# Optimization experiments

Measured on AMD Instinct MI355X. Metric: run time of the kernel, lower is better.

The kernel has to match this reference:

```python
import jax, jax.numpy as jnp
import numpy as np
from jax import lax

N_QUBITS = 8
N_BLOCKS = 5

_H = jnp.array([[1.0, 1.0], [1.0, -1.0]], dtype=jnp.complex64) / np.sqrt(2.0).astype(np.float32)
# torchquantum PauliY.diagonalizing_gates = [Z, S, H] applied in order -> matrix H @ S @ Z = H @ diag(1, -1j)
_YROT = _H @ jnp.diag(jnp.array([1.0, -1j], dtype=jnp.complex64))


def apply_gate(st, U, wires):
    # st: [N, 2, 2, ..., 2] (n_qubits trailing axes); U: [2^k, 2^k]
    k = len(wires)
    axes = [w + 1 for w in wires]
    s = jnp.moveaxis(st, axes, list(range(1, k + 1)))
    shp = s.shape
    s = s.reshape(shp[0], 2 ** k, -1)
    s = jnp.einsum('ij,bjr->bir', U, s)
    return jnp.moveaxis(s.reshape(shp), list(range(1, k + 1)), axes)


def u3_mat(th, ph, lam):
    c = jnp.cos(0.5 * th).astype(jnp.complex64)
    s = jnp.sin(0.5 * th).astype(jnp.complex64)
    el = jnp.exp(1j * lam)
    ep = jnp.exp(1j * ph)
    return jnp.stack([jnp.stack([c, -el * s]), jnp.stack([ep * s, ep * el * c])])


def cu3_mat(th, ph, lam):
    M = jnp.eye(4, dtype=jnp.complex64)
    return M.at[2:, 2:].set(u3_mat(th, ph, lam))


def z_expvals(st):
    # <Z_w> for every wire from marginal probabilities
    n = st.ndim - 1
    mag = st.real ** 2 + st.imag ** 2
    outs = []
    for w in range(n):
        axes = tuple(a for a in range(1, n + 1) if a != w + 1)
        p = mag.sum(axes)  # [N, 2]
        outs.append(p[:, 0] - p[:, 1])
    return jnp.stack(outs, axis=1)


def quantum_conv(x, conv_w, conv_b, u3_params, cu3_params, fc_w, fc_b):
    n = N_QUBITS
    B, C, H, W = x.shape
    y = lax.conv_general_dilated(x, conv_w, (1, 1), 'SAME',
                                 dimension_numbers=('NCHW', 'OIHW', 'NCHW'))
    y = y + conv_b[None, :, None, None]
    ang = y.transpose(0, 2, 3, 1).reshape(-1, n)  # [B*H*W, n_qubits]
    Npx = ang.shape[0]
    # RY(theta)|0> encoding: product state of [cos(t/2), sin(t/2)] per wire
    c = jnp.cos(0.5 * ang)
    s = jnp.sin(0.5 * ang)
    st = jnp.stack([c[:, 0], s[:, 0]], axis=1).astype(jnp.complex64)
    for w in range(1, n):
        q = jnp.stack([c[:, w], s[:, w]], axis=1).astype(jnp.complex64)
        st = (st[:, :, None] * q[:, None, :]).reshape(Npx, -1)
    st = st.reshape((Npx,) + (2,) * n)
    # U3CU3Layer0: per block, U3 on each wire then circular CU3 ring
    for b in range(N_BLOCKS):
        for w in range(n):
            st = apply_gate(st, u3_mat(u3_params[b, w, 0], u3_params[b, w, 1], u3_params[b, w, 2]), [w])
        for w in range(n):
            st = apply_gate(st, cu3_mat(cu3_params[b, w, 0], cu3_params[b, w, 1], cu3_params[b, w, 2]), [w, (w + 1) % n])
    # MeasureAll(Z), then MeasureAll(X) and MeasureAll(Y) which MUTATE the device
    # state with their diagonalizing gates (torchquantum semantics)
    mz = z_expvals(st)
    for w in range(n):
        st = apply_gate(st, _H, [w])
    mx = z_expvals(st)
    for w in range(n):
        st = apply_gate(st, _YROT, [w])
    my = z_expvals(st)
    meas = jnp.concatenate([mz, mx, my], axis=1)  # [B*H*W, 3*n]
    out = meas @ fc_w.T + fc_b
    return out.reshape(B, H, W, -1).transpose(0, 3, 1, 2)


def setup_inputs() -> dict:
    key = jax.random.key(0)
    ks = jax.random.split(key, 7)
    n, cin, cout = N_QUBITS, 16, 32
    x = jax.random.normal(ks[0], (4, cin, 64, 64), dtype=jnp.float32)
    conv_w = jax.random.normal(ks[1], (n, cin, 3, 3), dtype=jnp.float32) / np.sqrt(cin * 9)
    conv_b = jax.random.normal(ks[2], (n,), dtype=jnp.float32) * 0.01
    u3_params = jax.random.uniform(ks[3], (N_BLOCKS, n, 3), dtype=jnp.float32, minval=-np.pi, maxval=np.pi)
    cu3_params = jax.random.uniform(ks[4], (N_BLOCKS, n, 3), dtype=jnp.float32, minval=-np.pi, maxval=np.pi)
    fc_w = jax.random.normal(ks[5], (cout, 3 * n), dtype=jnp.float32) / np.sqrt(3 * n)
    fc_b = jax.random.normal(ks[6], (cout,), dtype=jnp.float32) * 0.01
    return {'x': x, 'conv_w': conv_w, 'conv_b': conv_b, 'u3_params': u3_params,
            'cu3_params': cu3_params, 'fc_w': fc_w, 'fc_b': fc_b}


def reference(x, conv_w, conv_b, u3_params, cu3_params, fc_w, fc_b):
    return quantum_conv(x, conv_w, conv_b, u3_params, cu3_params, fc_w, fc_b)
```

## Files before the change

kernel.cpp:

```cpp
#include <hip/hip_runtime.h>

typedef float v2f __attribute__((ext_vector_type(2)));

template<int C>
__device__ __forceinline__ float dppmov(float x) {
  return __int_as_float(__builtin_amdgcn_update_dpp(0, __float_as_int(x), C, 0xF, 0xF, true));
}
template<int IMM>
__device__ __forceinline__ float dswz(float x) {
  return __int_as_float(__builtin_amdgcn_ds_swizzle(__float_as_int(x), IMM));
}
__device__ __forceinline__ float bperm(float x, int a) {
  return __int_as_float(__builtin_amdgcn_ds_bpermute(a, __float_as_int(x)));
}
template<int M>
__device__ __forceinline__ float bfly(float x) {
  if constexpr (M == 1)      return dppmov<0xB1>(x);
  else if constexpr (M == 2) return dppmov<0x4E>(x);
  else if constexpr (M == 3) return dppmov<0x1B>(x);
  else if constexpr (M == 8) return dppmov<0x128>(x);
  else                       return dswz<0x101F>(x);
}
template<int M>
__device__ __forceinline__ v2f bfly2(v2f v) {
  v2f o; o.x = bfly<M>(v.x); o.y = bfly<M>(v.y); return o;
}
__device__ __forceinline__ v2f sp(float s) { v2f v; v.x = s; v.y = s; return v; }
__device__ __forceinline__ v2f vfma(v2f a, v2f b, v2f c) {
  return __builtin_elementwise_fma(a, b, c);
}

template<int M, int CM>
__device__ __forceinline__ void crossG(v2f Sr[16], v2f Si[16],
    const float* g, int lane) {
  const bool hi = (lane & M) != 0;
  float fr, fi, gr, gi;
  if constexpr (CM == 0) {
    fr = hi ? g[6] : g[0]; fi = hi ? g[7] : g[1];
    gr = hi ? g[4] : g[2]; gi = hi ? g[5] : g[3];
  } else {
    const bool ct = (lane & CM) != 0;
    float f0r = hi ? g[6]  : g[0],  f0i = hi ? g[7]  : g[1];
    float g0r = hi ? g[4]  : g[2],  g0i = hi ? g[5]  : g[3];
    float f1r = hi ? g[14] : g[8],  f1i = hi ? g[15] : g[9];
    float g1r = hi ? g[12] : g[10], g1i = hi ? g[13] : g[11];
    fr = ct ? f1r : f0r; fi = ct ? f1i : f0i;
    gr = ct ? g1r : g0r; gi = ct ? g1i : g0i;
  }
  v2f vfr = sp(fr), vfi = sp(fi), vgr = sp(gr), vgi = sp(gi);
  v2f vfiN = sp(-fi), vgiN = sp(-gi);
#pragma unroll
  for (int r = 0; r < 16; ++r) {
    v2f pR = bfly2<M>(Sr[r]);
    v2f pI = bfly2<M>(Si[r]);
    v2f nR = vfma(vgiN, pI, vfma(vgr, pR, vfma(vfiN, Si[r], vfr * Sr[r])));
    v2f nI = vfma(vgi,  pR, vfma(vgr, pI, vfma(vfi,  Sr[r], vfr * Si[r])));
    Sr[r] = nR; Si[r] = nI;
  }
}

__device__ __forceinline__ void mixP(v2f& x0r, v2f& x0i, v2f& x1r, v2f& x1i,
    float m0r, float m0i, float m1r, float m1i,
    float m2r, float m2i, float m3r, float m3i) {
  v2f n0r = vfma(sp(-m1i), x1i, vfma(sp(m1r), x1r, vfma(sp(-m0i), x0i, sp(m0r) * x0r)));
  v2f n0i = vfma(sp( m1i), x1r, vfma(sp(m1r), x1i, vfma(sp( m0i), x0r, sp(m0r) * x0i)));
  v2f n1r = vfma(sp(-m3i), x1i, vfma(sp(m3r), x1r, vfma(sp(-m2i), x0i, sp(m2r) * x0r)));
  v2f n1i = vfma(sp( m3i), x1r, vfma(sp(m3r), x1i, vfma(sp( m2i), x0r, sp(m2r) * x0i)));
  x0r = n0r; x0i = n0i; x1r = n1r; x1i = n1i;
}

__device__ __forceinline__ void f23N(v2f Sr[16], v2f Si[16],
    const float* tab, int lane) {
  const int idx = ((lane >> 2) & 1) * 4 + (lane & 3);
  const float* rp = tab + idx * 8;
  const float c0r = rp[0], c0i = rp[1], c1r = rp[2], c1i = rp[3];
  const float c2r = rp[4], c2i = rp[5], c3r = rp[6], c3i = rp[7];
#pragma unroll
  for (int r = 0; r < 16; ++r) {
    v2f p1R = bfly2<1>(Sr[r]), p1I = bfly2<1>(Si[r]);
    v2f p2R = bfly2<2>(Sr[r]), p2I = bfly2<2>(Si[r]);
    v2f p3R = bfly2<3>(Sr[r]), p3I = bfly2<3>(Si[r]);
    v2f nR = sp(c0r) * Sr[r];
    nR = vfma(sp(-c0i), Si[r], nR);
    nR = vfma(sp( c1r), p1R, nR);  nR = vfma(sp(-c1i), p1I, nR);
    nR = vfma(sp( c2r), p2R, nR);  nR = vfma(sp(-c2i), p2I, nR);
    nR = vfma(sp( c3r), p3R, nR);  nR = vfma(sp(-c3i), p3I, nR);
    v2f nI = sp(c0i) * Sr[r];
    nI = vfma(sp(c0r), Si[r], nI);
    nI = vfma(sp(c1i), p1R, nI);   nI = vfma(sp(c1r), p1I, nI);
    nI = vfma(sp(c2i), p2R, nI);   nI = vfma(sp(c2r), p2I, nI);
    nI = vfma(sp(c3i), p3R, nI);   nI = vfma(sp(c3r), p3I, nI);
    Sr[r] = nR; Si[r] = nI;
  }
}

__device__ __forceinline__ void f4N(v2f Sr[16], v2f Si[16],
    const float* g, int lane) {
  const bool ct = (lane & 1) != 0;
  float m[8];
#pragma unroll
  for (int jj = 0; jj < 8; ++jj) m[jj] = ct ? g[8 + jj] : g[jj];
#pragma unroll
  for (int r = 0; r < 8; ++r)
    mixP(Sr[r], Si[r], Sr[r + 8], Si[r + 8],
         m[0], m[1], m[2], m[3], m[4], m[5], m[6], m[7]);
}
__device__ __forceinline__ void f5N(v2f Sr[16], v2f Si[16], const float* g) {
#pragma unroll
  for (int r = 0; r < 4; ++r)
    mixP(Sr[r], Si[r], Sr[r + 4], Si[r + 4],
         g[0], g[1], g[2], g[3], g[4], g[5], g[6], g[7]);
#pragma unroll
  for (int r = 8; r < 12; ++r)
    mixP(Sr[r], Si[r], Sr[r + 4], Si[r + 4],
         g[8], g[9], g[10], g[11], g[12], g[13], g[14], g[15]);
}
__device__ __forceinline__ void f67N(v2f Sr[16], v2f Si[16], const float* T) {
#pragma unroll
  for (int qd = 0; qd < 4; ++qd) {
    const int B = qd * 4;
    const float* M = T + (qd & 1) * 32;
    v2f ar0 = Sr[B+0], ai0 = Si[B+0], ar1 = Sr[B+1], ai1 = Si[B+1];
    v2f ar2 = Sr[B+2], ai2 = Si[B+2], ar3 = Sr[B+3], ai3 = Si[B+3];
#pragma unroll
    for (int rp = 0; rp < 4; ++rp) {
      const float* Mr = M + rp * 8;
      v2f nR = sp(Mr[0]) * ar0;
      nR = vfma(sp(-Mr[1]), ai0, nR);
      nR = vfma(sp( Mr[2]), ar1, nR);
      nR = vfma(sp(-Mr[3]), ai1, nR);
      nR = vfma(sp( Mr[4]), ar2, nR);
      nR = vfma(sp(-Mr[5]), ai2, nR);
      nR = vfma(sp( Mr[6]), ar3, nR);
      nR = vfma(sp(-Mr[7]), ai3, nR);
      v2f nI = sp(Mr[1]) * ar0;
      nI = vfma(sp(Mr[0]), ai0, nI);
      nI = vfma(sp(Mr[3]), ar1, nI);
      nI = vfma(sp(Mr[2]), ai1, nI);
      nI = vfma(sp(Mr[5]), ar2, nI);
      nI = vfma(sp(Mr[4]), ai2, nI);
      nI = vfma(sp(Mr[7]), ar3, nI);
      nI = vfma(sp(Mr[6]), ai3, nI);
      Sr[B + rp] = nR; Si[B + rp] = nI;
    }
  }
}
__device__ __forceinline__ void f8pN(v2f Sr[16], v2f Si[16],
    const float* g, int lane) {
  const bool hi = (lane & 8) != 0;
  float fr[2], fi[2], gr[2], gi[2];
  fr[0] = hi ? g[6]  : g[0];  fi[0] = hi ? g[7]  : g[1];
  gr[0] = hi ? g[4]  : g[2];  gi[0] = hi ? g[5]  : g[3];
  fr[1] = hi ? g[14] : g[8];  fi[1] = hi ? g[15] : g[9];
  gr[1] = hi ? g[12] : g[10]; gi[1] = hi ? g[13] : g[11];
#pragma unroll
  for (int r = 0; r < 16; ++r) {
    const int m = r & 1;
    v2f pR = bfly2<8>(Sr[r]);
    v2f pI = bfly2<8>(Si[r]);
    v2f nR = vfma(sp(-gi[m]), pI, vfma(sp(gr[m]), pR, vfma(sp(-fi[m]), Si[r], sp(fr[m]) * Sr[r])));
    v2f nI = vfma(sp( gi[m]), pR, vfma(sp(gr[m]), pI, vfma(sp( fi[m]), Sr[r], sp(fr[m]) * Si[r])));
    Sr[r] = nR; Si[r] = nI;
  }
}
__device__ __forceinline__ void f8N(v2f Sr[16], v2f Si[16],
    const float* g, int lane) {
  const bool hi = (lane & 8) != 0;
  const float fr = hi ? g[6] : g[0], fi = hi ? g[7] : g[1];
  const float gr = hi ? g[4] : g[2], gi = hi ? g[5] : g[3];
#pragma unroll
  for (int r = 1; r < 16; r += 2) {
    v2f pR = bfly2<8>(Sr[r]);
    v2f pI = bfly2<8>(Si[r]);
    v2f nR = vfma(sp(-gi), pI, vfma(sp(gr), pR, vfma(sp(-fi), Si[r], sp(fr) * Sr[r])));
    v2f nI = vfma(sp( gi), pR, vfma(sp(gr), pI, vfma(sp( fi), Sr[r], sp(fr) * Si[r])));
    Sr[r] = nR; Si[r] = nI;
  }
}

template<int M>
__device__ __forceinline__ void crossO(const v2f Sr[16], const v2f Si[16],
                                       v2f& re, v2f& im) {
  v2f r = sp(0.0f), i = sp(0.0f);
#pragma unroll
  for (int k = 0; k < 16; ++k) {
    v2f pr = bfly2<M>(Sr[k]);
    v2f pi = bfly2<M>(Si[k]);
    r = vfma(Sr[k], pr, r);
    r = vfma(Si[k], pi, r);
    i = vfma(Si[k], pr, i);
    i = vfma(-Sr[k], pi, i);
  }
  re = r; im = i;
}

__device__ __forceinline__ void mm2(const float* A, const float* B, float* D) {
  D[0] = A[0]*B[0] - A[1]*B[1] + A[2]*B[4] - A[3]*B[5];
  D[1] = A[0]*B[1] + A[1]*B[0] + A[2]*B[5] + A[3]*B[4];
  D[2] = A[0]*B[2] - A[1]*B[3] + A[2]*B[6] - A[3]*B[7];
  D[3] = A[0]*B[3] + A[1]*B[2] + A[2]*B[7] + A[3]*B[6];
  D[4] = A[4]*B[0] - A[5]*B[1] + A[6]*B[4] - A[7]*B[5];
  D[5] = A[4]*B[1] + A[5]*B[0] + A[6]*B[5] + A[7]*B[4];
  D[6] = A[4]*B[2] - A[5]*B[3] + A[6]*B[6] - A[7]*B[7];
  D[7] = A[4]*B[3] + A[5]*B[2] + A[6]*B[7] + A[7]*B[6];
}
__device__ __forceinline__ void u3fill(const float* src, float* o) {
  float th = src[0], ph = src[1], lam = src[2];
  float c = cosf(0.5f * th), s = sinf(0.5f * th);
  float cl = cosf(lam), sl = sinf(lam);
  float cp = cosf(ph), spv = sinf(ph);
  float cpl = cosf(ph + lam), spl = sinf(ph + lam);
  o[0] = c;        o[1] = 0.0f;
  o[2] = -cl * s;  o[3] = -sl * s;
  o[4] = cp * s;   o[5] = spv * s;
  o[6] = cpl * c;  o[7] = spl * c;
}

__global__ __launch_bounds__(256) void qconv_kernel(
    const float* __restrict__ x, const float* __restrict__ cw,
    const float* __restrict__ cb, const float* __restrict__ u3p,
    const float* __restrict__ cu3p, const float* __restrict__ fcw,
    const float* __restrict__ fcb, float* __restrict__ out) {
  __shared__ float Us[40][8];
  __shared__ float Cs[40][8];
  __shared__ float Gs[640];
  __shared__ float FCWs[768];
  __shared__ float F23t[320];
  __shared__ float F67t[320];

  {
    const int t = threadIdx.x;
    if (t < 40) u3fill(u3p + t * 3, Us[t]);
    if (t >= 64 && t < 104) u3fill(cu3p + (t - 64) * 3, Cs[t - 64]);
    for (int i = t; i < 768; i += 256) {
      int tt = i % 24;
      int stage = tt >> 3, w = tt & 7;
      float sc = (stage >= 1 && w >= 4) ? 2.0f : 1.0f;
      FCWs[i] = fcw[i] * sc;
    }
    __syncthreads();
    if (t == 0) {
#pragma unroll
      for (int j = 0; j < 8; ++j) Gs[j] = Us[0][j];
    } else if (t < 36) {
      int j = t - 1, b = j / 7, k = j % 7;
      float* dst = Gs + 8 + b * 112 + k * 16;
      const float* U = Us[b * 8 + k + 1];
      const float* C = Cs[b * 8 + k];
#pragma unroll
      for (int u = 0; u < 8; ++u) dst[u] = U[u];
      mm2(C, U, dst + 8);
    } else if (t < 40) {
      int b = t - 36;
      float* dst = Gs + 568 + b * 16;
      const float* U = Us[(b + 1) * 8];
      const float* C = Cs[b * 8 + 7];
#pragma unroll
      for (int u = 0; u < 8; ++u) dst[u] = U[u];
      mm2(U, C, dst + 8);
    } else if (t == 40) {
#pragma unroll
      for (int j = 0; j < 8; ++j) Gs[632 + j] = Cs[39][j];
    }
    __syncthreads();
    if (t < 40) {
      int b = t >> 3, idx = t & 7;
      int ct = idx >> 2, row = idx & 3;
      const float* M2 = Gs + 8 + b * 112 + 16 + ct * 8;
      int w2p = row >> 1, w3p = row & 1;
      const float* M3 = Gs + 8 + b * 112 + 32 + w2p * 8;
      float* dst = F23t + b * 64 + idx * 8;
#pragma unroll
      for (int k = 0; k < 4; ++k) {
        int w2 = w2p ^ (k >> 1), w3 = w3p ^ (k & 1);
        float a_r = M2[(w2p * 2 + w2) * 2], a_i = M2[(w2p * 2 + w2) * 2 + 1];
        float b_r = M3[(w3p * 2 + w3) * 2], b_i = M3[(w3p * 2 + w3) * 2 + 1];
        dst[k * 2]     = a_r * b_r - a_i * b_i;
        dst[k * 2 + 1] = a_r * b_i + a_i * b_r;
      }
    } else if (t >= 64 && t < 104) {
      int u = t - 64;
      int b = u >> 3, idx = u & 7;
      int ct = idx >> 2, rp = idx & 3;
      const float* M6 = Gs + 8 + b * 112 + 80 + ct * 8;
      int b1p = rp >> 1, b0p = rp & 1;
      const float* M7 = Gs + 8 + b * 112 + 96 + b1p * 8;
      float* dst = F67t + b * 64 + ct * 32 + rp * 8;
#pragma unroll
      for (int c = 0; c < 4; ++c) {
        int b1 = c >> 1, b0 = c & 1;
        float a_r = M6[(b1p * 2 + b1) * 2], a_i = M6[(b1p * 2 + b1) * 2 + 1];
        float b_r = M7[(b0p * 2 + b0) * 2], b_i = M7[(b0p * 2 + b0) * 2 + 1];
        dst[c * 2]     = a_r * b_r - a_i * b_i;
        dst[c * 2 + 1] = a_r * b_i + a_i * b_r;
      }
    }
    __syncthreads();
  }

  const int lane = threadIdx.x & 63;
  const int wid = __builtin_amdgcn_readfirstlane(
      (int)((blockIdx.x * blockDim.x + threadIdx.x) >> 6));
  const int p0 = wid * 8;
  const int q = lane & 15;

  float ang;
  {
    const int px = lane >> 3;
    const int oc = lane & 7;
    const int p  = p0 + px;
    const int b  = p >> 12;
    const int hh = (p >> 6) & 63;
    const int wim = p & 63;
    float acc = cb[oc];
#pragma unroll 4
    for (int ic = 0; ic < 16; ++ic) {
      const float* wp = cw + (oc * 16 + ic) * 9;
      const float* xp = x + (b * 16 + ic) * 4096;
#pragma unroll
      for (int kh = 0; kh < 3; ++kh) {
        int ih = hh + kh - 1;
        bool rok = (unsigned)ih < 64u;
        int ihc = rok ? ih : 0;
#pragma unroll
        for (int kw = 0; kw < 3; ++kw) {
          int iw = wim + kw - 1;
          bool ok = rok && ((unsigned)iw < 64u);
          int iwc = ((unsigned)iw < 64u) ? iw : 0;
          float xv = xp[ihc * 64 + iwc];
          acc = fmaf(ok ? xv : 0.0f, wp[kh * 3 + kw], acc);
        }
      }
    }
    ang = acc;
  }

  v2f Sr[16], Si[16];
  {
    const int gb = (lane & 48) << 2;
    float aA[8], aB[8];
#pragma unroll
    for (int w = 0; w < 8; ++w) {
      aA[w] = bperm(ang, gb + (w << 2));
      aB[w] = bperm(ang, gb + ((8 + w) << 2));
    }
    float cA[8], sA[8], cB[8], sB[8];
#pragma unroll
    for (int w = 0; w < 8; ++w) {
      __sincosf(0.5f * aA[w], &sA[w], &cA[w]);
      __sincosf(0.5f * aB[w], &sB[w], &cB[w]);
    }
    v2f c0; c0.x = cA[0]; c0.y = cB[0];
    v2f s0; s0.x = sA[0]; s0.y = sB[0];
    v2f c0r = vfma(sp(Gs[2]), s0, sp(Gs[0]) * c0);
    v2f c0i = vfma(sp(Gs[3]), s0, sp(Gs[1]) * c0);
    v2f s0r = vfma(sp(Gs[6]), s0, sp(Gs[4]) * c0);
    v2f s0i = vfma(sp(Gs[7]), s0, sp(Gs[5]) * c0);
    const bool w0 = (q & 8) != 0;
    v2f selR = w0 ? s0r : c0r;
    v2f selI = w0 ? s0i : c0i;
    float fA = ((q & 4) ? sA[1] : cA[1]) * ((q & 2) ? sA[2] : cA[2])
             * ((q & 1) ? sA[3] : cA[3]);
    float fB = ((q & 4) ? sB[1] : cB[1]) * ((q & 2) ? sB[2] : cB[2])
             * ((q & 1) ? sB[3] : cB[3]);
    v2f uu[4], vv[4];
    uu[0].x = cA[6]*cA[7]; uu[1].x = cA[6]*sA[7];
    uu[2].x = sA[6]*cA[7]; uu[3].x = sA[6]*sA[7];
    uu[0].y = cB[6]*cB[7]; uu[1].y = cB[6]*sB[7];
    uu[2].y = sB[6]*cB[7]; uu[3].y = sB[6]*sB[7];
    float vA0 = fA * cA[4], vA1 = fA * sA[4];
    float vB0 = fB * cB[4], vB1 = fB * sB[4];
    vv[0].x = vA0*cA[5]; vv[1].x = vA0*sA[5];
    vv[2].x = vA1*cA[5]; vv[3].x = vA1*sA[5];
    vv[0].y = vB0*cB[5]; vv[1].y = vB0*sB[5];
    vv[2].y = vB1*cB[5]; vv[3].y = vB1*sB[5];
#pragma unroll
    for (int r = 0; r < 16; ++r) {
      v2f base = vv[r >> 2] * uu[r & 3];
      Sr[r] = selR * base;
      Si[r] = selI * base;
    }
  }

  for (int b = 0; b < 5; ++b) {
    const float* base = Gs + 8 + b * 112;
    crossG<4, 8>(Sr, Si, base + 0, lane);
    f23N(Sr, Si, F23t + b * 64, lane);
    f4N(Sr, Si, base + 48, lane);
    f5N(Sr, Si, base + 64);
    f67N(Sr, Si, F67t + b * 64);
    if (b < 4) f8pN(Sr, Si, Gs + 568 + b * 16, lane);
  }
  f8N(Sr, Si, Gs + 632, lane);

  float sg[4];
  sg[0] = (q & 8) ? -1.0f : 1.0f;
  sg[1] = (q & 4) ? -1.0f : 1.0f;
  sg[2] = (q & 2) ? -1.0f : 1.0f;
  sg[3] = (q & 1) ? -1.0f : 1.0f;

  v2f PT[24];
  {
    v2f re0, im0, re1, im1, re2, im2, re3, im3;
    crossO<8>(Sr, Si, re0, im0);
    crossO<4>(Sr, Si, re1, im1);
    crossO<2>(Sr, Si, re2, im2);
    crossO<1>(Sr, Si, re3, im3);
    PT[8]  = re0; PT[9]  = re1; PT[10] = re2; PT[11] = re3;
    PT[16] = sp(sg[0]) * im0; PT[17] = sp(sg[1]) * im1;
    PT[18] = sp(sg[2]) * im2; PT[19] = sp(sg[3]) * im3;

    v2f P[16];
#pragma unroll
    for (int r = 0; r < 16; ++r) P[r] = vfma(Si[r], Si[r], Sr[r] * Sr[r]);
    v2f t01[8];
#pragma unroll
    for (int k = 0; k < 8; ++k) t01[k] = P[2*k] + P[2*k+1];
    v2f q0 = t01[0] + t01[1], q1 = t01[2] + t01[3];
    v2f q2 = t01[4] + t01[5], q3 = t01[6] + t01[7];
    v2f h0 = q0 + q1, h1 = q2 + q3;
    v2f p  = h0 + h1;
    PT[4] = h0 - h1;
    PT[5] = (q0 - q1) + (q2 - q3);
    PT[6] = (t01[0]-t01[1]) + (t01[2]-t01[3])
          + (t01[4]-t01[5]) + (t01[6]-t01[7]);
    PT[7] = (P[0]-P[1]) + (P[2]-P[3]) + (P[4]-P[5]) + (P[6]-P[7])
          + (P[8]-P[9]) + (P[10]-P[11]) + (P[12]-P[13]) + (P[14]-P[15]);
    PT[0] = sp(sg[0]) * p; PT[1] = sp(sg[1]) * p;
    PT[2] = sp(sg[2]) * p; PT[3] = sp(sg[3]) * p;

    v2f re, im;
    re = sp(0.0f); im = sp(0.0f);
#pragma unroll
    for (int r = 0; r < 8; ++r) {
      re = vfma(Sr[r], Sr[r+8], re); re = vfma(Si[r], Si[r+8], re);
      im = vfma(Si[r], Sr[r+8], im); im = vfma(-Sr[r], Si[r+8], im);
    }
    PT[12] = re; PT[20] = im;
    re = sp(0.0f); im = sp(0.0f);
#pragma unroll
    for (int t = 0; t < 8; ++t) {
      const int lo = (t & 3) + (t >> 2) * 8;
      re = vfma(Sr[lo], Sr[lo+4], re); re = vfma(Si[lo], Si[lo+4], re);
      im = vfma(Si[lo], Sr[lo+4], im); im = vfma(-Sr[lo], Si[lo+4], im);
    }
    PT[13] = re; PT[21] = im;
    re = sp(0.0f); im = sp(0.0f);
#pragma unroll
    for (int t = 0; t < 8; ++t) {
      const int lo = (t & 1) + (t >> 1) * 4;
      re = vfma(Sr[lo], Sr[lo+2], re); re = vfma(Si[lo], Si[lo+2], re);
      im = vfma(Si[lo], Sr[lo+2], im); im = vfma(-Sr[lo], Si[lo+2], im);
    }
    PT[14] = re; PT[22] = im;
    re = sp(0.0f); im = sp(0.0f);
#pragma unroll
    for (int t = 0; t < 8; ++t) {
      const int lo = 2 * t;
      re = vfma(Sr[lo], Sr[lo+1], re); re = vfma(Si[lo], Si[lo+1], re);
      im = vfma(Si[lo], Sr[lo+1], im); im = vfma(-Sr[lo], Si[lo+1], im);
    }
    PT[15] = re; PT[23] = im;
  }

  const int j = q & 7;
  const bool isB = (q & 8) != 0;
  float mm[24];
#pragma unroll
  for (int t = 0; t < 24; ++t) {
    v2f v = PT[t] + bfly2<8>(PT[t]);
    float s = isB ? v.y : v.x;
    s += bfly<1>(s);
    s += bfly<2>(s);
    s += bfly<4>(s);
    mm[t] = s;
  }

  const int g = lane >> 4;
  const int p = p0 + 2 * g + (isB ? 1 : 0);
  const int ob = (p >> 12) * 131072 + (p & 4095);
#pragma unroll
  for (int k = 0; k < 4; ++k) {
    const int ch = 4 * j + k;
    const float* wr = FCWs + ch * 24;
    float acc = fcb[ch];
#pragma unroll
    for (int u = 0; u < 24; ++u) acc = fmaf(mm[u], wr[u], acc);
    out[ob + ch * 4096] = acc;
  }
}

extern "C" void kernel_launch(void* const* d_in, const int* in_sizes, int n_in,
                              void* d_out, int out_size, void* d_ws, size_t ws_size,
                              hipStream_t stream) {
  const float* x      = (const float*)d_in[0];
  const float* conv_w = (const float*)d_in[1];
  const float* conv_b = (const float*)d_in[2];
  const float* u3p    = (const float*)d_in[3];
  const float* cu3p   = (const float*)d_in[4];
  const float* fcw    = (const float*)d_in[5];
  const float* fcb    = (const float*)d_in[6];
  float* out = (float*)d_out;

  qconv_kernel<<<512, 256, 0, stream>>>(x, conv_w, conv_b, u3p, cu3p,
                                        fcw, fcb, out);
}
```

Baseline: 106.4 us.

## Split each pixel's statevector over 32 lanes instead of 16 to halve registers

Each wavefront now handles 4 pixels rather than 8, spreading every 256-amplitude state over 32 lanes with 8 packed register pairs. Qubit-to-lane mapping, butterfly masks, gate routines, conv split (two input-channel halves combined by a lane swap), measurement reductions and the FC weight layout are remapped to match, and the grid doubles to 1024 blocks with a waves-per-EU launch bound. Packed FMA/mul/add are forced through inline asm. The aim is lower register pressure and higher occupancy and parallelism, paid for with more cross-lane shuffles and an extra reduction step.

Result: slower. 115.0 us (+8.1%).

```diff
diff --git a/kernel.cpp b/kernel.cpp
--- a/kernel.cpp
+++ b/kernel.cpp
@@ -19,42 +19,53 @@
   else if constexpr (M == 2) return dppmov<0x4E>(x);
   else if constexpr (M == 3) return dppmov<0x1B>(x);
   else if constexpr (M == 8) return dppmov<0x128>(x);
-  else                       return dswz<0x101F>(x);
+  else if constexpr (M == 4) return dswz<0x101F>(x);
+  else                       return dswz<0x401F>(x);
 }
 template<int M>
 __device__ __forceinline__ v2f bfly2(v2f v) {
   v2f o; o.x = bfly<M>(v.x); o.y = bfly<M>(v.y); return o;
 }
 __device__ __forceinline__ v2f sp(float s) { v2f v; v.x = s; v.y = s; return v; }
+
 __device__ __forceinline__ v2f vfma(v2f a, v2f b, v2f c) {
-  return __builtin_elementwise_fma(a, b, c);
+  v2f d;
+  asm("v_pk_fma_f32 %0, %1, %2, %3" : "=v"(d) : "v"(a), "v"(b), "v"(c));
+  return d;
+}
+__device__ __forceinline__ v2f vmul2(v2f a, v2f b) {
+  v2f d;
+  asm("v_pk_mul_f32 %0, %1, %2" : "=v"(d) : "v"(a), "v"(b));
+  return d;
+}
+__device__ __forceinline__ v2f vadd2(v2f a, v2f b) {
+  v2f d;
+  asm("v_pk_add_f32 %0, %1, %2" : "=v"(d) : "v"(a), "v"(b));
+  return d;
+}
+__device__ __forceinline__ v2f vsub2(v2f a, v2f b) {
+  v2f r; r.x = a.x - b.x; r.y = a.y - b.y; return r;
 }
 
 template<int M, int CM>
-__device__ __forceinline__ void crossG(v2f Sr[16], v2f Si[16],
+__device__ __forceinline__ void crossG(v2f Sr[8], v2f Si[8],
     const float* g, int lane) {
   const bool hi = (lane & M) != 0;
-  float fr, fi, gr, gi;
-  if constexpr (CM == 0) {
-    fr = hi ? g[6] : g[0]; fi = hi ? g[7] : g[1];
-    gr = hi ? g[4] : g[2]; gi = hi ? g[5] : g[3];
-  } else {
-    const bool ct = (lane & CM) != 0;
-    float f0r = hi ? g[6]  : g[0],  f0i = hi ? g[7]  : g[1];
-    float g0r = hi ? g[4]  : g[2],  g0i = hi ? g[5]  : g[3];
-    float f1r = hi ? g[14] : g[8],  f1i = hi ? g[15] : g[9];
-    float g1r = hi ? g[12] : g[10], g1i = hi ? g[13] : g[11];
-    fr = ct ? f1r : f0r; fi = ct ? f1i : f0i;
-    gr = ct ? g1r : g0r; gi = ct ? g1i : g0i;
-  }
+  const bool ct = (lane & CM) != 0;
+  float f0r = hi ? g[6]  : g[0],  f0i = hi ? g[7]  : g[1];
+  float g0r = hi ? g[4]  : g[2],  g0i = hi ? g[5]  : g[3];
+  float f1r = hi ? g[14] : g[8],  f1i = hi ? g[15] : g[9];
+  float g1r = hi ? g[12] : g[10], g1i = hi ? g[13] : g[11];
+  float fr = ct ? f1r : f0r, fi = ct ? f1i : f0i;
+  float gr = ct ? g1r : g0r, gi = ct ? g1i : g0i;
   v2f vfr = sp(fr), vfi = sp(fi), vgr = sp(gr), vgi = sp(gi);
   v2f vfiN = sp(-fi), vgiN = sp(-gi);
 #pragma unroll
-  for (int r = 0; r < 16; ++r) {
+  for (int r = 0; r < 8; ++r) {
     v2f pR = bfly2<M>(Sr[r]);
     v2f pI = bfly2<M>(Si[r]);
-    v2f nR = vfma(vgiN, pI, vfma(vgr, pR, vfma(vfiN, Si[r], vfr * Sr[r])));
-    v2f nI = vfma(vgi,  pR, vfma(vgr, pI, vfma(vfi,  Sr[r], vfr * Si[r])));
+    v2f nR = vfma(vgiN, pI, vfma(vgr, pR, vfma(vfiN, Si[r], vmul2(vfr, Sr[r]))));
+    v2f nI = vfma(vgi,  pR, vfma(vgr, pI, vfma(vfi,  Sr[r], vmul2(vfr, Si[r]))));
     Sr[r] = nR; Si[r] = nI;
   }
 }
@@ -62,30 +73,30 @@
 __device__ __forceinline__ void mixP(v2f& x0r, v2f& x0i, v2f& x1r, v2f& x1i,
     float m0r, float m0i, float m1r, float m1i,
     float m2r, float m2i, float m3r, float m3i) {
-  v2f n0r = vfma(sp(-m1i), x1i, vfma(sp(m1r), x1r, vfma(sp(-m0i), x0i, sp(m0r) * x0r)));
-  v2f n0i = vfma(sp( m1i), x1r, vfma(sp(m1r), x1i, vfma(sp( m0i), x0r, sp(m0r) * x0i)));
-  v2f n1r = vfma(sp(-m3i), x1i, vfma(sp(m3r), x1r, vfma(sp(-m2i), x0i, sp(m2r) * x0r)));
-  v2f n1i = vfma(sp( m3i), x1r, vfma(sp(m3r), x1i, vfma(sp( m2i), x0r, sp(m2r) * x0i)));
+  v2f n0r = vfma(sp(-m1i), x1i, vfma(sp(m1r), x1r, vfma(sp(-m0i), x0i, vmul2(sp(m0r), x0r))));
+  v2f n0i = vfma(sp( m1i), x1r, vfma(sp(m1r), x1i, vfma(sp( m0i), x0r, vmul2(sp(m0r), x0i))));
+  v2f n1r = vfma(sp(-m3i), x1i, vfma(sp(m3r), x1r, vfma(sp(-m2i), x0i, vmul2(sp(m2r), x0r))));
+  v2f n1i = vfma(sp( m3i), x1r, vfma(sp(m3r), x1i, vfma(sp( m2i), x0r, vmul2(sp(m2r), x0i))));
   x0r = n0r; x0i = n0i; x1r = n1r; x1i = n1i;
 }
 
-__device__ __forceinline__ void f23N(v2f Sr[16], v2f Si[16],
+__device__ __forceinline__ void f23N(v2f Sr[8], v2f Si[8],
     const float* tab, int lane) {
-  const int idx = ((lane >> 2) & 1) * 4 + (lane & 3);
+  const int idx = ((lane >> 3) & 1) * 4 + (lane & 3);
   const float* rp = tab + idx * 8;
   const float c0r = rp[0], c0i = rp[1], c1r = rp[2], c1i = rp[3];
   const float c2r = rp[4], c2i = rp[5], c3r = rp[6], c3i = rp[7];
 #pragma unroll
-  for (int r = 0; r < 16; ++r) {
+  for (int r = 0; r < 8; ++r) {
     v2f p1R = bfly2<1>(Sr[r]), p1I = bfly2<1>(Si[r]);
     v2f p2R = bfly2<2>(Sr[r]), p2I = bfly2<2>(Si[r]);
     v2f p3R = bfly2<3>(Sr[r]), p3I = bfly2<3>(Si[r]);
-    v2f nR = sp(c0r) * Sr[r];
+    v2f nR = vmul2(sp(c0r), Sr[r]);
     nR = vfma(sp(-c0i), Si[r], nR);
     nR = vfma(sp( c1r), p1R, nR);  nR = vfma(sp(-c1i), p1I, nR);
     nR = vfma(sp( c2r), p2R, nR);  nR = vfma(sp(-c2i), p2I, nR);
     nR = vfma(sp( c3r), p3R, nR);  nR = vfma(sp(-c3i), p3I, nR);
-    v2f nI = sp(c0i) * Sr[r];
+    v2f nI = vmul2(sp(c0i), Sr[r]);
     nI = vfma(sp(c0r), Si[r], nI);
     nI = vfma(sp(c1i), p1R, nI);   nI = vfma(sp(c1r), p1I, nI);
     nI = vfma(sp(c2i), p2R, nI);   nI = vfma(sp(c2r), p2I, nI);
@@ -94,38 +105,28 @@
   }
 }
 
-__device__ __forceinline__ void f4N(v2f Sr[16], v2f Si[16],
-    const float* g, int lane) {
-  const bool ct = (lane & 1) != 0;
+__device__ __forceinline__ void f5N(v2f Sr[8], v2f Si[8], const float* g, int lane) {
+  const bool ct = (lane & 4) != 0;
   float m[8];
 #pragma unroll
   for (int jj = 0; jj < 8; ++jj) m[jj] = ct ? g[8 + jj] : g[jj];
-#pragma unroll
-  for (int r = 0; r < 8; ++r)
-    mixP(Sr[r], Si[r], Sr[r + 8], Si[r + 8],
-         m[0], m[1], m[2], m[3], m[4], m[5], m[6], m[7]);
-}
-__device__ __forceinline__ void f5N(v2f Sr[16], v2f Si[16], const float* g) {
 #pragma unroll
   for (int r = 0; r < 4; ++r)
     mixP(Sr[r], Si[r], Sr[r + 4], Si[r + 4],
-         g[0], g[1], g[2], g[3], g[4], g[5], g[6], g[7]);
-#pragma unroll
-  for (int r = 8; r < 12; ++r)
-    mixP(Sr[r], Si[r], Sr[r + 4], Si[r + 4],
-         g[8], g[9], g[10], g[11], g[12], g[13], g[14], g[15]);
-}
-__device__ __forceinline__ void f67N(v2f Sr[16], v2f Si[16], const float* T) {
-#pragma unroll
-  for (int qd = 0; qd < 4; ++qd) {
+         m[0], m[1], m[2], m[3], m[4], m[5], m[6], m[7]);
+}
+
+__device__ __forceinline__ void f67N(v2f Sr[8], v2f Si[8], const float* T) {
+#pragma unroll
+  for (int qd = 0; qd < 2; ++qd) {
     const int B = qd * 4;
-    const float* M = T + (qd & 1) * 32;
+    const float* M = T + qd * 32;
     v2f ar0 = Sr[B+0], ai0 = Si[B+0], ar1 = Sr[B+1], ai1 = Si[B+1];
     v2f ar2 = Sr[B+2], ai2 = Si[B+2], ar3 = Sr[B+3], ai3 = Si[B+3];
 #pragma unroll
     for (int rp = 0; rp < 4; ++rp) {
       const float* Mr = M + rp * 8;
-      v2f nR = sp(Mr[0]) * ar0;
+      v2f nR = vmul2(sp(Mr[0]), ar0);
       nR = vfma(sp(-Mr[1]), ai0, nR);
       nR = vfma(sp( Mr[2]), ar1, nR);
       nR = vfma(sp(-Mr[3]), ai1, nR);
@@ -133,7 +134,7 @@
       nR = vfma(sp(-Mr[5]), ai2, nR);
       nR = vfma(sp( Mr[6]), ar3, nR);
       nR = vfma(sp(-Mr[7]), ai3, nR);
-      v2f nI = sp(Mr[1]) * ar0;
+      v2f nI = vmul2(sp(Mr[1]), ar0);
       nI = vfma(sp(Mr[0]), ai0, nI);
       nI = vfma(sp(Mr[3]), ar1, nI);
       nI = vfma(sp(Mr[2]), ai1, nI);
@@ -145,53 +146,56 @@
     }
   }
 }
-__device__ __forceinline__ void f8pN(v2f Sr[16], v2f Si[16],
+
+__device__ __forceinline__ void f8pN(v2f Sr[8], v2f Si[8],
     const float* g, int lane) {
-  const bool hi = (lane & 8) != 0;
+  const bool hi = (lane & 16) != 0;
   float fr[2], fi[2], gr[2], gi[2];
   fr[0] = hi ? g[6]  : g[0];  fi[0] = hi ? g[7]  : g[1];
   gr[0] = hi ? g[4]  : g[2];  gi[0] = hi ? g[5]  : g[3];
   fr[1] = hi ? g[14] : g[8];  fi[1] = hi ? g[15] : g[9];
   gr[1] = hi ? g[12] : g[10]; gi[1] = hi ? g[13] : g[11];
 #pragma unroll
-  for (int r = 0; r < 16; ++r) {
+  for (int r = 0; r < 8; ++r) {
     const int m = r & 1;
-    v2f pR = bfly2<8>(Sr[r]);
-    v2f pI = bfly2<8>(Si[r]);
-    v2f nR = vfma(sp(-gi[m]), pI, vfma(sp(gr[m]), pR, vfma(sp(-fi[m]), Si[r], sp(fr[m]) * Sr[r])));
-    v2f nI = vfma(sp( gi[m]), pR, vfma(sp(gr[m]), pI, vfma(sp( fi[m]), Sr[r], sp(fr[m]) * Si[r])));
+    v2f pR = bfly2<16>(Sr[r]);
+    v2f pI = bfly2<16>(Si[r]);
+    v2f nR = vfma(sp(-gi[m]), pI, vfma(sp(gr[m]), pR, vfma(sp(-fi[m]), Si[r], vmul2(sp(fr[m]), Sr[r]))));
+    v2f nI = vfma(sp( gi[m]), pR, vfma(sp(gr[m]), pI, vfma(sp( fi[m]), Sr[r], vmul2(sp(fr[m]), Si[r]))));
     Sr[r] = nR; Si[r] = nI;
   }
 }
-__device__ __forceinline__ void f8N(v2f Sr[16], v2f Si[16],
+__device__ __forceinline__ void f8N(v2f Sr[8], v2f Si[8],
     const float* g, int lane) {
-  const bool hi = (lane & 8) != 0;
+  const bool hi = (lane & 16) != 0;
   const float fr = hi ? g[6] : g[0], fi = hi ? g[7] : g[1];
   const float gr = hi ? g[4] : g[2], gi = hi ? g[5] : g[3];
-#pragma unroll
-  for (int r = 1; r < 16; r += 2) {
-    v2f pR = bfly2<8>(Sr[r]);
-    v2f pI = bfly2<8>(Si[r]);
-    v2f nR = vfma(sp(-gi), pI, vfma(sp(gr), pR, vfma(sp(-fi), Si[r], sp(fr) * Sr[r])));
-    v2f nI = vfma(sp( gi), pR, vfma(sp(gr), pI, vfma(sp( fi), Sr[r], sp(fr) * Si[r])));
+  v2f vfr = sp(fr), vfi = sp(fi), vgr = sp(gr), vgi = sp(gi);
+  v2f vfiN = sp(-fi), vgiN = sp(-gi);
+#pragma unroll
+  for (int r = 1; r < 8; r += 2) {
+    v2f pR = bfly2<16>(Sr[r]);
+    v2f pI = bfly2<16>(Si[r]);
+    v2f nR = vfma(vgiN, pI, vfma(vgr, pR, vfma(vfiN, Si[r], vmul2(vfr, Sr[r]))));
+    v2f nI = vfma(vgi,  pR, vfma(vgr, pI, vfma(vfi,  Sr[r], vmul2(vfr, Si[r]))));
     Sr[r] = nR; Si[r] = nI;
   }
 }
 
 template<int M>
-__device__ __forceinline__ void crossO(const v2f Sr[16], const v2f Si[16],
+__device__ __forceinline__ void crossO(const v2f Sr[8], const v2f Si[8],
                                        v2f& re, v2f& im) {
-  v2f r = sp(0.0f), i = sp(0.0f);
-#pragma unroll
-  for (int k = 0; k < 16; ++k) {
+  v2f r = sp(0.0f), iP = sp(0.0f), iN = sp(0.0f);
+#pragma unroll
+  for (int k = 0; k < 8; ++k) {
     v2f pr = bfly2<M>(Sr[k]);
     v2f pi = bfly2<M>(Si[k]);
-    r = vfma(Sr[k], pr, r);
-    r = vfma(Si[k], pi, r);
-    i = vfma(Si[k], pr, i);
-    i = vfma(-Sr[k], pi, i);
-  }
-  re = r; im = i;
+    r  = vfma(Sr[k], pr, r);
+    r  = vfma(Si[k], pi, r);
+    iP = vfma(Si[k], pr, iP);
+    iN = vfma(Sr[k], pi, iN);
+  }
+  re = r; im = vsub2(iP, iN);
 }
 
 __device__ __forceinline__ void mm2(const float* A, const float* B, float* D) {
@@ -216,7 +220,7 @@
   o[6] = cpl * c;  o[7] = spl * c;
 }
 
-__global__ __launch_bounds__(256) void qconv_kernel(
+__global__ __launch_bounds__(256, 4) void qconv_kernel(
     const float* __restrict__ x, const float* __restrict__ cw,
     const float* __restrict__ cb, const float* __restrict__ u3p,
     const float* __restrict__ cu3p, const float* __restrict__ fcw,
@@ -233,10 +237,9 @@
     if (t < 40) u3fill(u3p + t * 3, Us[t]);
     if (t >= 64 && t < 104) u3fill(cu3p + (t - 64) * 3, Cs[t - 64]);
     for (int i = t; i < 768; i += 256) {
-      int tt = i % 24;
-      int stage = tt >> 3, w = tt & 7;
-      float sc = (stage >= 1 && w >= 4) ? 2.0f : 1.0f;
-      FCWs[i] = fcw[i] * sc;
+      int u = i >> 5, ch = i & 31;
+      float sc = (u >= 8 && (u & 7) >= 5) ? 2.0f : 1.0f;
+      FCWs[i] = fcw[ch * 24 + u] * sc;
     }
     __syncthreads();
     if (t == 0) {
@@ -301,20 +304,23 @@
   const int lane = threadIdx.x & 63;
   const int wid = __builtin_amdgcn_readfirstlane(
       (int)((blockIdx.x * blockDim.x + threadIdx.x) >> 6));
-  const int p0 = wid * 8;
-  const int q = lane & 15;
+  const int p0 = wid * 4;
+  const int q = lane & 31;
 
   float ang;
   {
-    const int px = lane >> 3;
+    const int px = lane >> 4;
     const int oc = lane & 7;
+    const int ichalf = (lane >> 3) & 1;
     const int p  = p0 + px;
     const int b  = p >> 12;
     const int hh = (p >> 6) & 63;
     const int wim = p & 63;
-    float acc = cb[oc];
+    float acc = ichalf ? 0.0f : cb[oc];
+    const int ic0 = ichalf * 8;
 #pragma unroll 4
-    for (int ic = 0; ic < 16; ++ic) {
+    for (int ici = 0; ici < 8; ++ici) {
+      const int ic = ic0 + ici;
       const float* wp = cw + (oc * 16 + ic) * 9;
       const float* xp = x + (b * 16 + ic) * 4096;
 #pragma unroll
@@ -332,17 +338,17 @@
         }
       }
     }
-    ang = acc;
-  }
-
-  v2f Sr[16], Si[16];
+    ang = acc + bfly<8>(acc);
+  }
+
+  v2f Sr[8], Si[8];
   {
-    const int gb = (lane & 48) << 2;
+    const int gb = lane & 32;
     float aA[8], aB[8];
 #pragma unroll
     for (int w = 0; w < 8; ++w) {
-      aA[w] = bperm(ang, gb + (w << 2));
-      aB[w] = bperm(ang, gb + ((8 + w) << 2));
+      aA[w] = bperm(ang, (gb + w) << 2);
+      aB[w] = bperm(ang, (gb + 16 + w) << 2);
     }
     float cA[8], sA[8], cB[8], sB[8];
 #pragma unroll
@@ -352,140 +358,131 @@
     }
     v2f c0; c0.x = cA[0]; c0.y = cB[0];
     v2f s0; s0.x = sA[0]; s0.y = sB[0];
-    v2f c0r = vfma(sp(Gs[2]), s0, sp(Gs[0]) * c0);
-    v2f c0i = vfma(sp(Gs[3]), s0, sp(Gs[1]) * c0);
-    v2f s0r = vfma(sp(Gs[6]), s0, sp(Gs[4]) * c0);
-    v2f s0i = vfma(sp(Gs[7]), s0, sp(Gs[5]) * c0);
-    const bool w0 = (q & 8) != 0;
+    v2f c0r = vfma(sp(Gs[2]), s0, vmul2(sp(Gs[0]), c0));
+    v2f c0i = vfma(sp(Gs[3]), s0, vmul2(sp(Gs[1]), c0));
+    v2f s0r = vfma(sp(Gs[6]), s0, vmul2(sp(Gs[4]), c0));
+    v2f s0i = vfma(sp(Gs[7]), s0, vmul2(sp(Gs[5]), c0));
+    const bool w0 = (q & 16) != 0;
     v2f selR = w0 ? s0r : c0r;
     v2f selI = w0 ? s0i : c0i;
-    float fA = ((q & 4) ? sA[1] : cA[1]) * ((q & 2) ? sA[2] : cA[2])
-             * ((q & 1) ? sA[3] : cA[3]);
-    float fB = ((q & 4) ? sB[1] : cB[1]) * ((q & 2) ? sB[2] : cB[2])
-             * ((q & 1) ? sB[3] : cB[3]);
-    v2f uu[4], vv[4];
+    float fA = ((q & 8) ? sA[1] : cA[1]) * ((q & 2) ? sA[2] : cA[2])
+             * ((q & 1) ? sA[3] : cA[3]) * ((q & 4) ? sA[4] : cA[4]);
+    float fB = ((q & 8) ? sB[1] : cB[1]) * ((q & 2) ? sB[2] : cB[2])
+             * ((q & 1) ? sB[3] : cB[3]) * ((q & 4) ? sB[4] : cB[4]);
+    v2f f; f.x = fA; f.y = fB;
+    selR = vmul2(selR, f);
+    selI = vmul2(selI, f);
+    v2f uu[4];
     uu[0].x = cA[6]*cA[7]; uu[1].x = cA[6]*sA[7];
     uu[2].x = sA[6]*cA[7]; uu[3].x = sA[6]*sA[7];
     uu[0].y = cB[6]*cB[7]; uu[1].y = cB[6]*sB[7];
     uu[2].y = sB[6]*cB[7]; uu[3].y = sB[6]*sB[7];
-    float vA0 = fA * cA[4], vA1 = fA * sA[4];
-    float vB0 = fB * cB[4], vB1 = fB * sB[4];
-    vv[0].x = vA0*cA[5]; vv[1].x = vA0*sA[5];
-    vv[2].x = vA1*cA[5]; vv[3].x = vA1*sA[5];
-    vv[0].y = vB0*cB[5]; vv[1].y = vB0*sB[5];
-    vv[2].y = vB1*cB[5]; vv[3].y = vB1*sB[5];
-#pragma unroll
-    for (int r = 0; r < 16; ++r) {
-      v2f base = vv[r >> 2] * uu[r & 3];
-      Sr[r] = selR * base;
-      Si[r] = selI * base;
+    v2f v5[2];
+    v5[0].x = cA[5]; v5[0].y = cB[5];
+    v5[1].x = sA[5]; v5[1].y = sB[5];
+#pragma unroll
+    for (int r = 0; r < 8; ++r) {
+      v2f base = vmul2(v5[r >> 2], uu[r & 3]);
+      Sr[r] = vmul2(selR, base);
+      Si[r] = vmul2(selI, base);
     }
   }
 
   for (int b = 0; b < 5; ++b) {
     const float* base = Gs + 8 + b * 112;
-    crossG<4, 8>(Sr, Si, base + 0, lane);
+    crossG<8, 16>(Sr, Si, base + 0, lane);
     f23N(Sr, Si, F23t + b * 64, lane);
-    f4N(Sr, Si, base + 48, lane);
-    f5N(Sr, Si, base + 64);
+    crossG<4, 1>(Sr, Si, base + 48, lane);
+    f5N(Sr, Si, base + 64, lane);
     f67N(Sr, Si, F67t + b * 64);
     if (b < 4) f8pN(Sr, Si, Gs + 568 + b * 16, lane);
   }
   f8N(Sr, Si, Gs + 632, lane);
 
-  float sg[4];
-  sg[0] = (q & 8) ? -1.0f : 1.0f;
-  sg[1] = (q & 4) ? -1.0f : 1.0f;
-  sg[2] = (q & 2) ? -1.0f : 1.0f;
-  sg[3] = (q & 1) ? -1.0f : 1.0f;
+  float sg[5];
+  sg[0] = (q & 16) ? -1.0f : 1.0f;
+  sg[1] = (q & 8)  ? -1.0f : 1.0f;
+  sg[2] = (q & 2)  ? -1.0f : 1.0f;
+  sg[3] = (q & 1)  ? -1.0f : 1.0f;
+  sg[4] = (q & 4)  ? -1.0f : 1.0f;
 
   v2f PT[24];
   {
-    v2f re0, im0, re1, im1, re2, im2, re3, im3;
-    crossO<8>(Sr, Si, re0, im0);
-    crossO<4>(Sr, Si, re1, im1);
-    crossO<2>(Sr, Si, re2, im2);
-    crossO<1>(Sr, Si, re3, im3);
-    PT[8]  = re0; PT[9]  = re1; PT[10] = re2; PT[11] = re3;
-    PT[16] = sp(sg[0]) * im0; PT[17] = sp(sg[1]) * im1;
-    PT[18] = sp(sg[2]) * im2; PT[19] = sp(sg[3]) * im3;
-
-    v2f P[16];
-#pragma unroll
-    for (int r = 0; r < 16; ++r) P[r] = vfma(Si[r], Si[r], Sr[r] * Sr[r]);
-    v2f t01[8];
-#pragma unroll
-    for (int k = 0; k < 8; ++k) t01[k] = P[2*k] + P[2*k+1];
-    v2f q0 = t01[0] + t01[1], q1 = t01[2] + t01[3];
-    v2f q2 = t01[4] + t01[5], q3 = t01[6] + t01[7];
-    v2f h0 = q0 + q1, h1 = q2 + q3;
-    v2f p  = h0 + h1;
-    PT[4] = h0 - h1;
-    PT[5] = (q0 - q1) + (q2 - q3);
-    PT[6] = (t01[0]-t01[1]) + (t01[2]-t01[3])
-          + (t01[4]-t01[5]) + (t01[6]-t01[7]);
-    PT[7] = (P[0]-P[1]) + (P[2]-P[3]) + (P[4]-P[5]) + (P[6]-P[7])
-          + (P[8]-P[9]) + (P[10]-P[11]) + (P[12]-P[13]) + (P[14]-P[15]);
-    PT[0] = sp(sg[0]) * p; PT[1] = sp(sg[1]) * p;
-    PT[2] = sp(sg[2]) * p; PT[3] = sp(sg[3]) * p;
-
     v2f re, im;
-    re = sp(0.0f); im = sp(0.0f);
-#pragma unroll
-    for (int r = 0; r < 8; ++r) {
-      re = vfma(Sr[r], Sr[r+8], re); re = vfma(Si[r], Si[r+8], re);
-      im = vfma(Si[r], Sr[r+8], im); im = vfma(-Sr[r], Si[r+8], im);
-    }
-    PT[12] = re; PT[20] = im;
-    re = sp(0.0f); im = sp(0.0f);
-#pragma unroll
-    for (int t = 0; t < 8; ++t) {
-      const int lo = (t & 3) + (t >> 2) * 8;
-      re = vfma(Sr[lo], Sr[lo+4], re); re = vfma(Si[lo], Si[lo+4], re);
-      im = vfma(Si[lo], Sr[lo+4], im); im = vfma(-Sr[lo], Si[lo+4], im);
-    }
-    PT[13] = re; PT[21] = im;
-    re = sp(0.0f); im = sp(0.0f);
-#pragma unroll
-    for (int t = 0; t < 8; ++t) {
+    crossO<16>(Sr, Si, re, im); PT[8]  = re; PT[16] = vmul2(sp(sg[0]), im);
+    crossO<8>(Sr, Si, re, im);  PT[9]  = re; PT[17] = vmul2(sp(sg[1]), im);
+    crossO<2>(Sr, Si, re, im);  PT[10] = re; PT[18] = vmul2(sp(sg[2]), im);
+    crossO<1>(Sr, Si, re, im);  PT[11] = re; PT[19] = vmul2(sp(sg[3]), im);
+    crossO<4>(Sr, Si, re, im);  PT[12] = re; PT[20] = vmul2(sp(sg[4]), im);
+
+    v2f rA, iP, iN;
+    rA = sp(0.0f); iP = sp(0.0f); iN = sp(0.0f);
+#pragma unroll
+    for (int r = 0; r < 4; ++r) {
+      rA = vfma(Sr[r], Sr[r+4], rA); rA = vfma(Si[r], Si[r+4], rA);
+      iP = vfma(Si[r], Sr[r+4], iP); iN = vfma(Sr[r], Si[r+4], iN);
+    }
+    PT[13] = rA; PT[21] = vsub2(iP, iN);
+    rA = sp(0.0f); iP = sp(0.0f); iN = sp(0.0f);
+#pragma unroll
+    for (int t = 0; t < 4; ++t) {
       const int lo = (t & 1) + (t >> 1) * 4;
-      re = vfma(Sr[lo], Sr[lo+2], re); re = vfma(Si[lo], Si[lo+2], re);
-      im = vfma(Si[lo], Sr[lo+2], im); im = vfma(-Sr[lo], Si[lo+2], im);
-    }
-    PT[14] = re; PT[22] = im;
-    re = sp(0.0f); im = sp(0.0f);
-#pragma unroll
-    for (int t = 0; t < 8; ++t) {
+      rA = vfma(Sr[lo], Sr[lo+2], rA); rA = vfma(Si[lo], Si[lo+2], rA);
+      iP = vfma(Si[lo], Sr[lo+2], iP); iN = vfma(Sr[lo], Si[lo+2], iN);
+    }
+    PT[14] = rA; PT[22] = vsub2(iP, iN);
+    rA = sp(0.0f); iP = sp(0.0f); iN = sp(0.0f);
+#pragma unroll
+    for (int t = 0; t < 4; ++t) {
       const int lo = 2 * t;
-      re = vfma(Sr[lo], Sr[lo+1], re); re = vfma(Si[lo], Si[lo+1], re);
-      im = vfma(Si[lo], Sr[lo+1], im); im = vfma(-Sr[lo], Si[lo+1], im);
-    }
-    PT[15] = re; PT[23] = im;
-  }
-
-  const int j = q & 7;
-  const bool isB = (q & 8) != 0;
+      rA = vfma(Sr[lo], Sr[lo+1], rA); rA = vfma(Si[lo], Si[lo+1], rA);
+      iP = vfma(Si[lo], Sr[lo+1], iP); iN = vfma(Sr[lo], Si[lo+1], iN);
+    }
+    PT[15] = rA; PT[23] = vsub2(iP, iN);
+
+    v2f P[8];
+#pragma unroll
+    for (int r = 0; r < 8; ++r) P[r] = vfma(Si[r], Si[r], vmul2(Sr[r], Sr[r]));
+    v2f t01[4];
+#pragma unroll
+    for (int k = 0; k < 4; ++k) t01[k] = vadd2(P[2*k], P[2*k+1]);
+    v2f q0 = vadd2(t01[0], t01[1]), q1 = vadd2(t01[2], t01[3]);
+    v2f p  = vadd2(q0, q1);
+    PT[5] = vsub2(q0, q1);
+    PT[6] = vadd2(vsub2(t01[0], t01[1]), vsub2(t01[2], t01[3]));
+    PT[7] = vadd2(vadd2(vsub2(P[0], P[1]), vsub2(P[2], P[3])),
+                  vadd2(vsub2(P[4], P[5]), vsub2(P[6], P[7])));
+    PT[0] = vmul2(sp(sg[0]), p);
+    PT[1] = vmul2(sp(sg[1]), p);
+    PT[2] = vmul2(sp(sg[2]), p);
+    PT[3] = vmul2(sp(sg[3]), p);
+    PT[4] = vmul2(sp(sg[4]), p);
+  }
+
+  const int j = q & 15;
+  const bool isB = (q & 16) != 0;
   float mm[24];
 #pragma unroll
   for (int t = 0; t < 24; ++t) {
-    v2f v = PT[t] + bfly2<8>(PT[t]);
-    float s = isB ? v.y : v.x;
+    float own = isB ? PT[t].y : PT[t].x;
+    float oth = isB ? PT[t].x : PT[t].y;
+    float s = own + bfly<16>(oth);
     s += bfly<1>(s);
     s += bfly<2>(s);
     s += bfly<4>(s);
+    s += bfly<8>(s);
     mm[t] = s;
   }
 
-  const int g = lane >> 4;
+  const int g = lane >> 5;
   const int p = p0 + 2 * g + (isB ? 1 : 0);
   const int ob = (p >> 12) * 131072 + (p & 4095);
 #pragma unroll
-  for (int k = 0; k < 4; ++k) {
-    const int ch = 4 * j + k;
-    const float* wr = FCWs + ch * 24;
+  for (int k = 0; k < 2; ++k) {
+    const int ch = 2 * j + k;
     float acc = fcb[ch];
 #pragma unroll
-    for (int u = 0; u < 24; ++u) acc = fmaf(mm[u], wr[u], acc);
+    for (int u = 0; u < 24; ++u) acc = fmaf(mm[u], FCWs[u * 32 + ch], acc);
     out[ob + ch * 4096] = acc;
   }
 }
@@ -502,6 +499,6 @@
   const float* fcb    = (const float*)d_in[6];
   float* out = (float*)d_out;
 
-  qconv_kernel<<<512, 256, 0, stream>>>(x, conv_w, conv_b, u3p, cu3p,
-                                        fcw, fcb, out);
-}
+  qconv_kernel<<<1024, 256, 0, stream>>>(x, conv_w, conv_b, u3p, cu3p,
+                                         fcw, fcb, out);
+}
```
